# Kernel tuning notes

Measured on AMD Instinct MI355X. Metric: run time of the kernel, lower is better.

Reference implementation:

```python
import jax, jax.numpy as jnp
import numpy as np

B, S, D, H = 2, 2048, 1024, 16
DH = D // H  # 64


def setup_inputs() -> dict:
    key = jax.random.key(0)
    ks = jax.random.split(key, 9)
    s = 1.0 / np.sqrt(D)
    return {
        "x": jax.random.normal(ks[0], (B, S, D), dtype=jnp.float32),
        "Wq": jax.random.normal(ks[1], (D, D), dtype=jnp.float32) * s,
        "bq": jnp.zeros((D,), dtype=jnp.float32),
        "Wk": jax.random.normal(ks[2], (D, D), dtype=jnp.float32) * s,
        "bk": jnp.zeros((D,), dtype=jnp.float32),
        "Wv": jax.random.normal(ks[3], (D, D), dtype=jnp.float32) * s,
        "bv": jnp.zeros((D,), dtype=jnp.float32),
        "Wo": jax.random.normal(ks[4], (D, D), dtype=jnp.float32) * s,
        "bo": jnp.zeros((D,), dtype=jnp.float32),
    }


def _split_heads(t):
    # [B, S, D] -> [B, H, S, DH]
    return t.reshape(B, S, H, DH).transpose(0, 2, 1, 3)


def reference(x, Wq, bq, Wk, bk, Wv, bv, Wo, bo):
    q = _split_heads(x @ Wq + bq)
    k = _split_heads(x @ Wk + bk)
    v = _split_heads(x @ Wv + bv)
    scale = 1.0 / jnp.sqrt(jnp.asarray(DH, dtype=x.dtype))
    # [B, H, S, S] score matrix (materialized, as in the original)
    logits = jnp.einsum("bhqd,bhkd->bhqk", q, k) * scale
    attn = jax.nn.softmax(logits, axis=-1)
    out = jnp.einsum("bhqk,bhkd->bhqd", attn, v)
    out = out.transpose(0, 2, 1, 3).reshape(B, S, D)
    return out @ Wo + bo
```

## Files before the change

### kernel.cpp

```cpp
#include <hip/hip_runtime.h>
#include <hip/hip_bf16.h>
#include <stdint.h>


typedef __attribute__((ext_vector_type(8))) short bf16x8;
typedef __attribute__((ext_vector_type(4))) float f32x4;

__device__ __forceinline__ void gld16(const void* g, void* l) {
  __builtin_amdgcn_global_load_lds((const __attribute__((address_space(1))) void*)g,
                                   (__attribute__((address_space(3))) void*)l, 16, 0, 0);
}

__device__ __forceinline__ unsigned short f2b(float f) {
  __hip_bfloat16 h = __float2bfloat16(f);
  return *reinterpret_cast<unsigned short*>(&h);
}

__global__ __launch_bounds__(256) void prep_kernel(const float* __restrict__ x,
                                                   const float* __restrict__ Wq,
                                                   const float* __restrict__ Wk,
                                                   const float* __restrict__ Wv,
                                                   const float* __restrict__ Wo,
                                                   unsigned short* __restrict__ xb,
                                                   unsigned short* __restrict__ wt) {
  __shared__ unsigned short Ls[64 * 72];
  int bid = blockIdx.x;
  int t = threadIdx.x;
  if (bid < 4096) {
    int i = (bid * 256 + t) * 4;
    float4 v = *(const float4*)(x + i);
    ushort4 o = make_ushort4(f2b(v.x), f2b(v.y), f2b(v.z), f2b(v.w));
    *(ushort4*)(xb + i) = o;
    return;
  }
  int tid = bid - 4096;
  int z = tid >> 8, rem = tid & 255;
  int bx = rem & 15, by = rem >> 4;
  const float* src = (z == 0) ? Wq : (z == 1) ? Wk : (z == 2) ? Wv : Wo;
  unsigned short* dst = wt + (size_t)z * 1024 * 1024;
  int k0 = bx * 64, n0 = by * 64;
  int c4 = t & 15;
#pragma unroll
  for (int it = 0; it < 4; ++it) {
    int row = it * 16 + (t >> 4);
    float4 v = *(const float4*)(src + (k0 + row) * 1024 + n0 + c4 * 4);
    Ls[(c4 * 4 + 0) * 72 + row] = f2b(v.x);
    Ls[(c4 * 4 + 1) * 72 + row] = f2b(v.y);
    Ls[(c4 * 4 + 2) * 72 + row] = f2b(v.z);
    Ls[(c4 * 4 + 3) * 72 + row] = f2b(v.w);
  }
  __syncthreads();
  int nr = t >> 2, kc = (t & 3) * 16;
  *(uint4*)(dst + (size_t)(n0 + nr) * 1024 + k0 + kc) = *(uint4*)&Ls[nr * 72 + kc];
  *(uint4*)(dst + (size_t)(n0 + nr) * 1024 + k0 + kc + 8) = *(uint4*)&Ls[nr * 72 + kc + 8];
}

__global__ __launch_bounds__(256) void gemm_qkv(const unsigned short* __restrict__ Ab,
                                                const unsigned short* __restrict__ Bt,
                                                const float* __restrict__ bq,
                                                const float* __restrict__ bk,
                                                const float* __restrict__ bv,
                                                unsigned short* __restrict__ qb,
                                                unsigned short* __restrict__ kb,
                                                unsigned short* __restrict__ vtb) {
  __shared__ unsigned short As[128 * 32];
  __shared__ unsigned short Bs[128 * 32];
  __shared__ unsigned short Es[128 * 72];
  const int t = threadIdx.x;
  const int lane = t & 63, wave = t >> 6;
  const int m0 = blockIdx.x * 128, n0 = blockIdx.y * 128;
  const int wr = (wave >> 1) * 64, wc = (wave & 1) * 64;
  const int fr = lane & 15, fq = lane >> 4;
  f32x4 acc[4][4] = {};
  for (int kt = 0; kt < 32; ++kt) {
    const unsigned short* Ag = Ab + (size_t)m0 * 1024 + kt * 32;
    const unsigned short* Bg = Bt + (size_t)n0 * 1024 + kt * 32;
#pragma unroll
    for (int rep = 0; rep < 2; ++rep) {
      int c = t + rep * 256;
      int row = c >> 2, col = (c & 3) * 8;
      gld16(Ag + (size_t)row * 1024 + col, (void*)(As + c * 8));
      gld16(Bg + (size_t)row * 1024 + col, (void*)(Bs + c * 8));
    }
    __syncthreads();
    bf16x8 a[4], b[4];
#pragma unroll
    for (int i = 0; i < 4; ++i) a[i] = *(const bf16x8*)&As[(wr + i * 16 + fr) * 32 + fq * 8];
#pragma unroll
    for (int j = 0; j < 4; ++j) b[j] = *(const bf16x8*)&Bs[(wc + j * 16 + fr) * 32 + fq * 8];
#pragma unroll
    for (int i = 0; i < 4; ++i)
#pragma unroll
      for (int j = 0; j < 4; ++j)
        acc[i][j] = __builtin_amdgcn_mfma_f32_16x16x32_bf16(a[i], b[j], acc[i][j], 0, 0, 0);
    __syncthreads();
  }
  const int which = n0 >> 10;
  const int bidx = m0 >> 11, s0 = m0 & 2047;
  if (which == 2) {
#pragma unroll
    for (int nh = 0; nh < 2; ++nh) {
      if ((wc >> 6) == nh) {
#pragma unroll
        for (int j = 0; j < 4; ++j) {
          int col = j * 16 + fr;
          float bias = bv[(n0 + nh * 64 + col) & 1023];
#pragma unroll
          for (int i = 0; i < 4; ++i) {
            int sl = wr + i * 16 + fq * 4;
            ushort4 pk;
            pk.x = f2b(acc[i][j][0] + bias);
            pk.y = f2b(acc[i][j][1] + bias);
            pk.z = f2b(acc[i][j][2] + bias);
            pk.w = f2b(acc[i][j][3] + bias);
            *(uint2*)&Es[col * 136 + sl] = *(uint2*)&pk;
          }
        }
      }
      __syncthreads();
      int h = ((n0 + nh * 64) & 1023) >> 6;
#pragma unroll
      for (int it = 0; it < 4; ++it) {
        int dh = it * 16 + (t >> 4);
        int ck = (t & 15) * 8;
        uint4 vv = *(uint4*)&Es[dh * 136 + ck];
        *(uint4*)&vtb[(size_t)((bidx * 16 + h) * 64 + dh) * 2048 + s0 + ck] = vv;
      }
      __syncthreads();
    }
  } else {
    unsigned short* dst = (which == 0) ? qb : kb;
    const float* bias_p = (which == 0) ? bq : bk;
    float scale = (which == 0) ? 0.1803368801111204f : 1.0f;
#pragma unroll
    for (int nh = 0; nh < 2; ++nh) {
      if ((wc >> 6) == nh) {
#pragma unroll
        for (int j = 0; j < 4; ++j) {
          int col = j * 16 + fr;
          float bias = bias_p[(n0 + nh * 64 + col) & 1023];
#pragma unroll
          for (int i = 0; i < 4; ++i)
#pragma unroll
            for (int r = 0; r < 4; ++r) {
              int sl = wr + i * 16 + fq * 4 + r;
              Es[sl * 72 + col] = f2b((acc[i][j][r] + bias) * scale);
            }
        }
      }
      __syncthreads();
      int h = ((n0 + nh * 64) & 1023) >> 6;
#pragma unroll
      for (int it = 0; it < 4; ++it) {
        int sl = it * 32 + (t >> 3);
        int ck = (t & 7) * 8;
        uint4 vv = *(uint4*)&Es[sl * 72 + ck];
        *(uint4*)&dst[(size_t)((bidx * 16 + h) * 2048 + s0 + sl) * 64 + ck] = vv;
      }
      __syncthreads();
    }
  }
}

__global__ __launch_bounds__(256, 2) void attn_kernel(const unsigned short* __restrict__ qb,
                                                      const unsigned short* __restrict__ kb,
                                                      const unsigned short* __restrict__ vtb,
                                                      unsigned short* __restrict__ attn) {
  __shared__ unsigned short Ks[2 * 4096];
  __shared__ unsigned short Vs[2 * 4096];
  __shared__ unsigned short Ps[4 * 1024];
  const int t = threadIdx.x, lane = t & 63, w = t >> 6;
  const int fr = lane & 15, fq = lane >> 4;
  const int rid = blockIdx.y * 32 + blockIdx.x;
  const int bh = (rid & 7) + ((rid >> 8) << 3);
  const int q0 = ((rid >> 3) & 31) * 64;
  const int ksel = (fq ^ ((fr >> 1) & 3)) * 8;
  const unsigned short* qg = qb + (size_t)bh * 2048 * 64;
  const unsigned short* kg0 = kb + (size_t)bh * 2048 * 64;
  const unsigned short* vg0 = vtb + (size_t)bh * 64 * 2048;

  bf16x8 qf[2];
#pragma unroll
  for (int kk = 0; kk < 2; ++kk)
    qf[kk] = *(const bf16x8*)(qg + (size_t)(q0 + w * 16 + fr) * 64 + kk * 32 + fq * 8);

  bf16x8 ones;
#pragma unroll
  for (int i = 0; i < 8; ++i) ones[i] = (short)0x3F80;

  f32x4 oacc[4] = {};
  f32x4 lacc = {};
  unsigned short* Pw = Ps + w * 1024;

  {
#pragma unroll
    for (int rep = 0; rep < 2; ++rep) {
      int c = t + rep * 256;
      int kk = c >> 8, row = (c >> 2) & 63, cc = c & 3;
      int cs = cc ^ ((row >> 1) & 3);
      gld16(kg0 + row * 64 + kk * 32 + cs * 8, (void*)(Ks + c * 8));
      gld16(vg0 + (size_t)row * 2048 + kk * 32 + cs * 8, (void*)(Vs + c * 8));
    }
  }

  for (int kt = 0; kt < 32; ++kt) {
    int buf = kt & 1;
    __syncthreads();
    if (kt + 1 < 32) {
      const unsigned short* kg = kg0 + (size_t)(kt + 1) * 4096;
      const unsigned short* vg = vg0 + (kt + 1) * 64;
      int lb = (buf ^ 1) * 4096;
#pragma unroll
      for (int rep = 0; rep < 2; ++rep) {
        int c = t + rep * 256;
        int kk = c >> 8, row = (c >> 2) & 63, cc = c & 3;
        int cs = cc ^ ((row >> 1) & 3);
        gld16(kg + row * 64 + kk * 32 + cs * 8, (void*)(Ks + lb + c * 8));
        gld16(vg + (size_t)row * 2048 + kk * 32 + cs * 8, (void*)(Vs + lb + c * 8));
      }
    }
    const unsigned short* Kb = Ks + buf * 4096;
    const unsigned short* Vb = Vs + buf * 4096;
    f32x4 sacc[4] = {};
#pragma unroll
    for (int kk = 0; kk < 2; ++kk) {
      bf16x8 kf[4];
#pragma unroll
      for (int m = 0; m < 4; ++m) kf[m] = *(const bf16x8*)&Kb[kk * 2048 + (m * 16 + fr) * 32 + ksel];
      __builtin_amdgcn_s_setprio(1);
#pragma unroll
      for (int m = 0; m < 4; ++m)
        sacc[m] = __builtin_amdgcn_mfma_f32_16x16x32_bf16(kf[m], qf[kk], sacc[m], 0, 0, 0);
      __builtin_amdgcn_s_setprio(0);
    }
#pragma unroll
    for (int m = 0; m < 4; ++m) {
      int G = (m * 2 + (fq >> 1)) ^ (fr & 7);
      ushort4 pk;
      pk.x = f2b(__builtin_amdgcn_exp2f(sacc[m][0]));
      pk.y = f2b(__builtin_amdgcn_exp2f(sacc[m][1]));
      pk.z = f2b(__builtin_amdgcn_exp2f(sacc[m][2]));
      pk.w = f2b(__builtin_amdgcn_exp2f(sacc[m][3]));
      *(uint2*)&Pw[fr * 64 + G * 8 + (fq & 1) * 4] = *(uint2*)&pk;
    }
#pragma unroll
    for (int kk = 0; kk < 2; ++kk) {
      int G = (kk * 4 + fq) ^ (fr & 7);
      bf16x8 pf = *(const bf16x8*)&Pw[fr * 64 + G * 8];
      __builtin_amdgcn_s_setprio(1);
#pragma unroll
      for (int n = 0; n < 4; ++n) {
        bf16x8 vf = *(const bf16x8*)&Vb[kk * 2048 + (n * 16 + fr) * 32 + ksel];
        oacc[n] = __builtin_amdgcn_mfma_f32_16x16x32_bf16(pf, vf, oacc[n], 0, 0, 0);
      }
      lacc = __builtin_amdgcn_mfma_f32_16x16x32_bf16(pf, ones, lacc, 0, 0, 0);
      __builtin_amdgcn_s_setprio(0);
    }
  }
  int bidx = bh >> 4, h = bh & 15;
#pragma unroll
  for (int r = 0; r < 4; ++r) {
    float inv = 1.f / lacc[r];
    int s = q0 + w * 16 + fq * 4 + r;
    size_t base = (size_t)(bidx * 2048 + s) * 1024 + h * 64;
#pragma unroll
    for (int n = 0; n < 4; ++n) attn[base + n * 16 + fr] = f2b(oacc[n][r] * inv);
  }
}

__global__ __launch_bounds__(256) void gemm_out(const unsigned short* __restrict__ Ab,
                                                const unsigned short* __restrict__ Bt,
                                                const float* __restrict__ bo,
                                                float* __restrict__ out) {
  __shared__ unsigned short As[128 * 32];
  __shared__ unsigned short Bs[128 * 32];
  const int t = threadIdx.x;
  const int lane = t & 63, wave = t >> 6;
  const int m0 = blockIdx.x * 128, n0 = blockIdx.y * 128;
  const int wr = (wave >> 1) * 64, wc = (wave & 1) * 64;
  const int fr = lane & 15, fq = lane >> 4;
  f32x4 acc[4][4] = {};
  for (int kt = 0; kt < 32; ++kt) {
    const unsigned short* Ag = Ab + (size_t)m0 * 1024 + kt * 32;
    const unsigned short* Bg = Bt + (size_t)n0 * 1024 + kt * 32;
#pragma unroll
    for (int rep = 0; rep < 2; ++rep) {
      int c = t + rep * 256;
      int row = c >> 2, col = (c & 3) * 8;
      gld16(Ag + (size_t)row * 1024 + col, (void*)(As + c * 8));
      gld16(Bg + (size_t)row * 1024 + col, (void*)(Bs + c * 8));
    }
    __syncthreads();
    bf16x8 a[4], b[4];
#pragma unroll
    for (int i = 0; i < 4; ++i) a[i] = *(const bf16x8*)&As[(wr + i * 16 + fr) * 32 + fq * 8];
#pragma unroll
    for (int j = 0; j < 4; ++j) b[j] = *(const bf16x8*)&Bs[(wc + j * 16 + fr) * 32 + fq * 8];
#pragma unroll
    for (int i = 0; i < 4; ++i)
#pragma unroll
      for (int j = 0; j < 4; ++j)
        acc[i][j] = __builtin_amdgcn_mfma_f32_16x16x32_bf16(a[i], b[j], acc[i][j], 0, 0, 0);
    __syncthreads();
  }
#pragma unroll
  for (int j = 0; j < 4; ++j) {
    int gn = n0 + wc + j * 16 + fr;
    float bias = bo[gn];
#pragma unroll
    for (int i = 0; i < 4; ++i)
#pragma unroll
      for (int r = 0; r < 4; ++r) {
        int gm = m0 + wr + i * 16 + fq * 4 + r;
        out[(size_t)gm * 1024 + gn] = acc[i][j][r] + bias;
      }
  }
}

extern "C" void kernel_launch(void* const* d_in, const int* in_sizes, int n_in,
                              void* d_out, int out_size, void* d_ws, size_t ws_size,
                              hipStream_t stream) {
  const float* x = (const float*)d_in[0];
  const float* Wq = (const float*)d_in[1];
  const float* bq = (const float*)d_in[2];
  const float* Wk = (const float*)d_in[3];
  const float* bk = (const float*)d_in[4];
  const float* Wv = (const float*)d_in[5];
  const float* bv = (const float*)d_in[6];
  const float* Wo = (const float*)d_in[7];
  const float* bo = (const float*)d_in[8];
  float* out = (float*)d_out;

  unsigned short* ws = (unsigned short*)d_ws;
  const size_t MI = (size_t)1024 * 1024;
  unsigned short* xb = ws;
  unsigned short* wt = ws + 4 * MI;
  unsigned short* qb = wt + 4 * MI;
  unsigned short* kb = qb + 4 * MI;
  unsigned short* vtb = kb + 4 * MI;
  unsigned short* attn = xb;

  prep_kernel<<<5120, 256, 0, stream>>>(x, Wq, Wk, Wv, Wo, xb, wt);
  gemm_qkv<<<dim3(32, 24), 256, 0, stream>>>(xb, wt, bq, bk, bv, qb, kb, vtb);
  attn_kernel<<<dim3(32, 32), 256, 0, stream>>>(qb, kb, vtb, attn);
  gemm_out<<<dim3(32, 8), 256, 0, stream>>>(attn, wt + 3 * MI, bo, out);
}
```

Measured before the change: 209.3 us.

## Switch attention to 32x32x16 MFMA with 128-query blocks and scalar row sums

The attention kernel now uses 32x32x16 bf16 MFMA tiles, with each wave handling 32 query rows, so a block covers 128 queries and the grid is halved. The softmax denominator is accumulated with scalar adds of the exponentials plus a cross-half shuffle, replacing the extra MFMA against a ones vector. Reciprocals are shared through LDS for the final write. The aim is to reuse each K/V tile across more queries and cut MFMA issue count. The cost is more registers and LDS per block, and only 512 blocks may leave CUs underfilled.

```diff
diff --git a/kernel.cpp b/kernel.cpp
--- a/kernel.cpp
+++ b/kernel.cpp
@@ -5,6 +5,7 @@
 
 typedef __attribute__((ext_vector_type(8))) short bf16x8;
 typedef __attribute__((ext_vector_type(4))) float f32x4;
+typedef __attribute__((ext_vector_type(16))) float f32x16;
 
 __device__ __forceinline__ void gld16(const void* g, void* l) {
   __builtin_amdgcn_global_load_lds((const __attribute__((address_space(1))) void*)g,
@@ -168,29 +169,26 @@
                                                       unsigned short* __restrict__ attn) {
   __shared__ unsigned short Ks[2 * 4096];
   __shared__ unsigned short Vs[2 * 4096];
-  __shared__ unsigned short Ps[4 * 1024];
+  __shared__ unsigned short Ps[4 * 2048];
+  __shared__ float Linv[4][32];
   const int t = threadIdx.x, lane = t & 63, w = t >> 6;
-  const int fr = lane & 15, fq = lane >> 4;
-  const int rid = blockIdx.y * 32 + blockIdx.x;
-  const int bh = (rid & 7) + ((rid >> 8) << 3);
-  const int q0 = ((rid >> 3) & 31) * 64;
-  const int ksel = (fq ^ ((fr >> 1) & 3)) * 8;
+  const int qh = lane & 31, hi = lane >> 5;
+  const int rid = blockIdx.y * 16 + blockIdx.x;
+  const int bh = (rid & 7) + ((rid >> 7) << 3);
+  const int q0 = ((rid >> 3) & 15) * 128;
   const unsigned short* qg = qb + (size_t)bh * 2048 * 64;
   const unsigned short* kg0 = kb + (size_t)bh * 2048 * 64;
   const unsigned short* vg0 = vtb + (size_t)bh * 64 * 2048;
 
-  bf16x8 qf[2];
-#pragma unroll
-  for (int kk = 0; kk < 2; ++kk)
-    qf[kk] = *(const bf16x8*)(qg + (size_t)(q0 + w * 16 + fr) * 64 + kk * 32 + fq * 8);
-
-  bf16x8 ones;
-#pragma unroll
-  for (int i = 0; i < 8; ++i) ones[i] = (short)0x3F80;
-
-  f32x4 oacc[4] = {};
-  f32x4 lacc = {};
-  unsigned short* Pw = Ps + w * 1024;
+  bf16x8 qf[4];
+#pragma unroll
+  for (int st = 0; st < 4; ++st)
+    qf[st] = *(const bf16x8*)(qg + (size_t)(q0 + w * 32 + qh) * 64 + st * 16 + hi * 8);
+
+  f32x16 oacc[2] = {};
+  float lsum = 0.f;
+  char* PwB = (char*)Ps + w * 4096;
+  const int swz = (qh & 7) << 4;
 
   {
 #pragma unroll
@@ -221,50 +219,58 @@
     }
     const unsigned short* Kb = Ks + buf * 4096;
     const unsigned short* Vb = Vs + buf * 4096;
-    f32x4 sacc[4] = {};
-#pragma unroll
-    for (int kk = 0; kk < 2; ++kk) {
-      bf16x8 kf[4];
-#pragma unroll
-      for (int m = 0; m < 4; ++m) kf[m] = *(const bf16x8*)&Kb[kk * 2048 + (m * 16 + fr) * 32 + ksel];
-      __builtin_amdgcn_s_setprio(1);
-#pragma unroll
-      for (int m = 0; m < 4; ++m)
-        sacc[m] = __builtin_amdgcn_mfma_f32_16x16x32_bf16(kf[m], qf[kk], sacc[m], 0, 0, 0);
-      __builtin_amdgcn_s_setprio(0);
-    }
-#pragma unroll
-    for (int m = 0; m < 4; ++m) {
-      int G = (m * 2 + (fq >> 1)) ^ (fr & 7);
-      ushort4 pk;
-      pk.x = f2b(__builtin_amdgcn_exp2f(sacc[m][0]));
-      pk.y = f2b(__builtin_amdgcn_exp2f(sacc[m][1]));
-      pk.z = f2b(__builtin_amdgcn_exp2f(sacc[m][2]));
-      pk.w = f2b(__builtin_amdgcn_exp2f(sacc[m][3]));
-      *(uint2*)&Pw[fr * 64 + G * 8 + (fq & 1) * 4] = *(uint2*)&pk;
-    }
-#pragma unroll
-    for (int kk = 0; kk < 2; ++kk) {
-      int G = (kk * 4 + fq) ^ (fr & 7);
-      bf16x8 pf = *(const bf16x8*)&Pw[fr * 64 + G * 8];
-      __builtin_amdgcn_s_setprio(1);
-#pragma unroll
-      for (int n = 0; n < 4; ++n) {
-        bf16x8 vf = *(const bf16x8*)&Vb[kk * 2048 + (n * 16 + fr) * 32 + ksel];
-        oacc[n] = __builtin_amdgcn_mfma_f32_16x16x32_bf16(pf, vf, oacc[n], 0, 0, 0);
-      }
-      lacc = __builtin_amdgcn_mfma_f32_16x16x32_bf16(pf, ones, lacc, 0, 0, 0);
-      __builtin_amdgcn_s_setprio(0);
-    }
-  }
+    f32x16 sacc[2] = {};
+    __builtin_amdgcn_s_setprio(1);
+#pragma unroll
+    for (int st = 0; st < 4; ++st) {
+#pragma unroll
+      for (int m = 0; m < 2; ++m) {
+        int s = m * 32 + qh;
+        int cs = ((st & 1) * 2 + hi) ^ ((s >> 1) & 3);
+        bf16x8 kf = *(const bf16x8*)&Kb[(st >> 1) * 2048 + s * 32 + cs * 8];
+        sacc[m] = __builtin_amdgcn_mfma_f32_32x32x16_bf16(kf, qf[st], sacc[m], 0, 0, 0);
+      }
+    }
+    __builtin_amdgcn_s_setprio(0);
+#pragma unroll
+    for (int m = 0; m < 2; ++m)
+#pragma unroll
+      for (int g = 0; g < 4; ++g) {
+        float e0 = __builtin_amdgcn_exp2f(sacc[m][g * 4 + 0]);
+        float e1 = __builtin_amdgcn_exp2f(sacc[m][g * 4 + 1]);
+        float e2 = __builtin_amdgcn_exp2f(sacc[m][g * 4 + 2]);
+        float e3 = __builtin_amdgcn_exp2f(sacc[m][g * 4 + 3]);
+        lsum += (e0 + e1) + (e2 + e3);
+        ushort4 pk = make_ushort4(f2b(e0), f2b(e1), f2b(e2), f2b(e3));
+        int kbyte = m * 64 + g * 16 + hi * 8;
+        *(uint2*)(PwB + qh * 128 + (kbyte ^ swz)) = *(uint2*)&pk;
+      }
+    __builtin_amdgcn_s_setprio(1);
+#pragma unroll
+    for (int st = 0; st < 4; ++st) {
+      int kbyte = st * 32 + hi * 16;
+      bf16x8 pf = *(const bf16x8*)(PwB + qh * 128 + (kbyte ^ swz));
+#pragma unroll
+      for (int n = 0; n < 2; ++n) {
+        int dh = n * 32 + qh;
+        int cs = ((st & 1) * 2 + hi) ^ ((dh >> 1) & 3);
+        bf16x8 vf = *(const bf16x8*)&Vb[(st >> 1) * 2048 + dh * 32 + cs * 8];
+        oacc[n] = __builtin_amdgcn_mfma_f32_32x32x16_bf16(pf, vf, oacc[n], 0, 0, 0);
+      }
+    }
+    __builtin_amdgcn_s_setprio(0);
+  }
+  lsum += __shfl_xor(lsum, 32);
+  Linv[w][qh] = 1.f / lsum;
   int bidx = bh >> 4, h = bh & 15;
 #pragma unroll
-  for (int r = 0; r < 4; ++r) {
-    float inv = 1.f / lacc[r];
-    int s = q0 + w * 16 + fq * 4 + r;
+  for (int r = 0; r < 16; ++r) {
+    int qloc = (r & 3) + 8 * (r >> 2) + 4 * hi;
+    float iv = Linv[w][qloc];
+    int s = q0 + w * 32 + qloc;
     size_t base = (size_t)(bidx * 2048 + s) * 1024 + h * 64;
 #pragma unroll
-    for (int n = 0; n < 4; ++n) attn[base + n * 16 + fr] = f2b(oacc[n][r] * inv);
+    for (int n = 0; n < 2; ++n) attn[base + n * 32 + qh] = f2b(oacc[n][r] * iv);
   }
 }
 
@@ -342,6 +348,6 @@
 
   prep_kernel<<<5120, 256, 0, stream>>>(x, Wq, Wk, Wv, Wo, xb, wt);
   gemm_qkv<<<dim3(32, 24), 256, 0, stream>>>(xb, wt, bq, bk, bv, qb, kb, vtb);
-  attn_kernel<<<dim3(32, 32), 256, 0, stream>>>(qb, kb, vtb, attn);
+  attn_kernel<<<dim3(16, 32), 256, 0, stream>>>(qb, kb, vtb, attn);
   gemm_out<<<dim3(32, 8), 256, 0, stream>>>(attn, wt + 3 * MI, bo, out);
 }
```

Result: no change. 208.9 us (-0.2%).
